# Kernel tuning notes

Measured on AMD Instinct MI355X. Metric: run time of the kernel, lower is better.

## Reference

```python
import jax, jax.numpy as jnp
from jax import lax
import numpy as np

B, H, W, C = 32, 56, 56, 384
NH, WS, SS = 12, 7, 3
HD = C // NH
N = WS * WS
HID = 384  # int(mlp_ratio*dim / reduce_scale) = int(4*384/4)
SCALE = HD ** -0.5
L = H * W


def _rel_pos_index():
    coords = np.stack(np.meshgrid(np.arange(WS), np.arange(WS), indexing='ij'))
    cf = coords.reshape(2, -1)
    rc = (cf[:, :, None] - cf[:, None, :]).transpose(1, 2, 0)
    rc[..., 0] += WS - 1
    rc[..., 1] += WS - 1
    rc[..., 0] *= 2 * WS - 1
    return rc.sum(-1).reshape(-1)  # (N*N,)


def _win_part_np(x):
    b, h, w, c = x.shape
    x = x.reshape(b, h // WS, WS, w // WS, WS, c).transpose(0, 1, 3, 2, 4, 5)
    return x.reshape(-1, WS, WS, c)


def _attn_mask():
    img = np.zeros((1, H, W, 1), np.float32)
    cnt = 0
    sl = (slice(0, -WS), slice(-WS, -SS), slice(-SS, None))
    for hs in sl:
        for ws in sl:
            img[:, hs, ws, :] = cnt
            cnt += 1
    mw = _win_part_np(img).reshape(-1, N)
    am = mw[:, None, :] - mw[:, :, None]
    return np.where(am != 0, -100.0, 0.0).astype(np.float32)  # (nW, N, N)


REL_IDX = _rel_pos_index()
ATTN_MASK = _attn_mask()


def window_partition(x):  # (B,H,W,C) -> (B*nW, N, C)
    x = x.reshape(B, H // WS, WS, W // WS, WS, C).transpose(0, 1, 3, 2, 4, 5)
    return x.reshape(-1, N, C)


def window_reverse(wins):  # (B*nW, N, C) -> (B,H,W,C)
    x = wins.reshape(B, H // WS, W // WS, WS, WS, C).transpose(0, 1, 3, 2, 4, 5)
    return x.reshape(B, H, W, C)


def _ln(x, g, b):
    m = x.mean(-1, keepdims=True)
    v = ((x - m) ** 2).mean(-1, keepdims=True)
    return (x - m) * lax.rsqrt(v + 1e-5) * g + b


def setup_inputs() -> dict:
    key = jax.random.key(0)
    ks = iter(jax.random.split(key, 16))
    w = lambda shape: jax.random.normal(next(ks), shape, jnp.float32) * 0.02
    return {
        'x': jax.random.normal(next(ks), (B, L, C), jnp.float32),
        'norm1_g': jnp.ones((C,), jnp.float32), 'norm1_b': jnp.zeros((C,), jnp.float32),
        'qkv_w': w((3 * C, C)), 'qkv_b': jnp.zeros((3 * C,), jnp.float32),
        'rpb_table': w(((2 * WS - 1) ** 2, NH)),
        'proj_w': w((C, C)), 'proj_b': jnp.zeros((C,), jnp.float32),
        'se1_w': w((C // 2, C)), 'se1_b': jnp.zeros((C // 2,), jnp.float32),
        'se2_w': w((C, C // 2)), 'se2_b': jnp.zeros((C,), jnp.float32),
        'norm2_g': jnp.ones((C,), jnp.float32), 'norm2_b': jnp.zeros((C,), jnp.float32),
        'c1_w': w((HID, C)), 'c1_b': jnp.zeros((HID,), jnp.float32),
        'bn1_g': jnp.ones((HID,), jnp.float32), 'bn1_b': jnp.zeros((HID,), jnp.float32),
        'dw_w': w((HID, 1, 3, 3)), 'dw_b': jnp.zeros((HID,), jnp.float32),
        'bn2_g': jnp.ones((HID,), jnp.float32), 'bn2_b': jnp.zeros((HID,), jnp.float32),
        'c2_w': w((C, HID)), 'c2_b': jnp.zeros((C,), jnp.float32),
        'bn3_g': jnp.ones((C,), jnp.float32), 'bn3_b': jnp.zeros((C,), jnp.float32),
    }


def reference(x, norm1_g, norm1_b, qkv_w, qkv_b, rpb_table, proj_w, proj_b,
              se1_w, se1_b, se2_w, se2_b, norm2_g, norm2_b,
              c1_w, c1_b, bn1_g, bn1_b, dw_w, dw_b, bn2_g, bn2_b,
              c2_w, c2_b, bn3_g, bn3_b):
    shortcut = x
    h = _ln(x, norm1_g, norm1_b).reshape(B, H, W, C)
    h = jnp.roll(h, (-SS, -SS), axis=(1, 2))           # cyclic shift (SW-MSA)
    win = window_partition(h)                            # (B*nW, N, C)
    qkv = (win @ qkv_w.T + qkv_b).reshape(-1, N, 3, NH, HD).transpose(2, 0, 3, 1, 4)
    q, k, v = qkv[0] * SCALE, qkv[1], qkv[2]             # (B*nW, NH, N, HD)
    attn = jnp.einsum('bhnd,bhmd->bhnm', q, k)           # (B*nW, NH, N, N)
    rpb = rpb_table[jnp.asarray(REL_IDX)].reshape(N, N, NH).transpose(2, 0, 1)
    attn = attn + rpb[None]
    mask = jnp.asarray(ATTN_MASK)                        # (nW, N, N)
    nW = mask.shape[0]
    attn = (attn.reshape(B, nW, NH, N, N) + mask[None, :, None]).reshape(-1, NH, N, N)
    attn = jax.nn.softmax(attn, axis=-1)
    out = jnp.einsum('bhnm,bhmd->bhnd', attn, v).transpose(0, 2, 1, 3).reshape(-1, N, C)
    out = out @ proj_w.T + proj_b
    h = window_reverse(out)
    h = jnp.roll(h, (SS, SS), axis=(1, 2)).reshape(B, L, C)
    x = shortcut + h
    # SE gating, applied token-wise over channel dim exactly as ChannelSELayer_SA
    g = jax.nn.relu(x @ se1_w.T + se1_b)
    g = jax.nn.sigmoid(g @ se2_w.T + se2_b)
    x = x * g
    # light conv MLP branch (Mlp_Light); BatchNorm in eval mode with running
    # mean 0 / var 1 -> pure per-channel affine
    y = _ln(x, norm2_g, norm2_b).reshape(B, H, W, C).transpose(0, 3, 1, 2)  # NCHW
    y = jnp.einsum('bchw,oc->bohw', y, c1_w) + c1_b[None, :, None, None]     # 1x1 conv
    y = jax.nn.gelu(y, approximate=False) * bn1_g[None, :, None, None] + bn1_b[None, :, None, None]
    y = lax.conv_general_dilated(y, dw_w, (1, 1), 'SAME', feature_group_count=HID,
                                 dimension_numbers=('NCHW', 'OIHW', 'NCHW')) + dw_b[None, :, None, None]
    y = jax.nn.gelu(y, approximate=False) * bn2_g[None, :, None, None] + bn2_b[None, :, None, None]
    y = jnp.einsum('bchw,oc->bohw', y, c2_w) + c2_b[None, :, None, None]     # 1x1 conv
    y = y * bn3_g[None, :, None, None] + bn3_b[None, :, None, None]
    x = x + y.transpose(0, 2, 3, 1).reshape(B, L, C)
    return x
```

## Files before the change

### kernel.cpp

```cpp
#include <hip/hip_runtime.h>
#include <hip/hip_bf16.h>

typedef __attribute__((ext_vector_type(4))) float f32x4;
typedef __attribute__((ext_vector_type(8))) __bf16 bf16x8;
typedef __attribute__((ext_vector_type(8))) unsigned short u16x8;

#define SCALE_ 0.17677669529663687f
#define RS 19267584

#define OFF_R1 77070336ull
#define OFF_WB 154140672ull
#define OFF_WT 156205056ull

__device__ __forceinline__ __bf16 tobf(float f) {
  __hip_bfloat16 h = __float2bfloat16(f);
  return __builtin_bit_cast(__bf16, h);
}
__device__ __forceinline__ unsigned short f2u(float f) {
  return __builtin_bit_cast(unsigned short, __float2bfloat16(f));
}

__global__ __launch_bounds__(256) void cvt_kernel(const float* __restrict__ src,
                                                  __hip_bfloat16* __restrict__ dst, int n) {
  int i = blockIdx.x * 256 + threadIdx.x;
  int stride = gridDim.x * 256;
  for (; i < n; i += stride) dst[i] = __float2bfloat16(src[i]);
}

__global__ __launch_bounds__(256) void dwrep_kernel(const float* __restrict__ src,
                                                    float* __restrict__ dst) {
  int i = blockIdx.x * 256 + threadIdx.x;
  if (i < 3456) {
    int c = i / 9, k = i - c * 9;
    dst[k * 384 + c] = src[i];
  }
}

template <bool WIN>
__global__ __launch_bounds__(256) void ln_kernel(const float* __restrict__ x,
                                                 const float* __restrict__ gm,
                                                 const float* __restrict__ bt,
                                                 __hip_bfloat16* __restrict__ out) {
  const int tok = blockIdx.x * 4 + (threadIdx.x >> 6);
  const int lane = threadIdx.x & 63;
  const float2* row = (const float2*)(x + (size_t)tok * 384);
  float2 v[3];
  v[0] = row[lane]; v[1] = row[lane + 64]; v[2] = row[lane + 128];
  float s = 0.f, sq = 0.f;
#pragma unroll
  for (int i = 0; i < 3; ++i) { s += v[i].x + v[i].y; sq += v[i].x * v[i].x + v[i].y * v[i].y; }
#pragma unroll
  for (int m = 1; m < 64; m <<= 1) { s += __shfl_xor(s, m, 64); sq += __shfl_xor(sq, m, 64); }
  const float mean = s * (1.f / 384.f);
  const float var = sq * (1.f / 384.f) - mean * mean;
  const float rstd = rsqrtf(var + 1e-5f);
  size_t dst;
  if constexpr (WIN) {
    int b = tok / 3136, l = tok - b * 3136;
    int i = l / 56, j = l - i * 56;
    int hp = i - 3; if (hp < 0) hp += 56;
    int wp = j - 3; if (wp < 0) wp += 56;
    int wi = (hp / 7) * 8 + wp / 7;
    int n = (hp % 7) * 7 + wp % 7;
    dst = (size_t)(b * 64 + wi) * 49 + n;
  } else {
    dst = (size_t)tok;
  }
  unsigned int* o = (unsigned int*)(out + dst * 384);
  const float2* G = (const float2*)gm;
  const float2* Bv = (const float2*)bt;
#pragma unroll
  for (int i = 0; i < 3; ++i) {
    int j = lane + 64 * i;
    float2 gv = G[j], bv = Bv[j];
    float a = (v[i].x - mean) * rstd * gv.x + bv.x;
    float b2 = (v[i].y - mean) * rstd * gv.y + bv.y;
    o[j] = (unsigned)f2u(a) | ((unsigned)f2u(b2) << 16);
  }
}

enum { EPI_PROJ = 0, EPI_SE2 = 2, EPI_C1 = 3, EPI_C2 = 4, EPI_QKV = 5 };

template <int EPI, int KD>
__global__ __launch_bounds__(256) void gemm5(const __hip_bfloat16* __restrict__ Ap,
                                             const __hip_bfloat16* __restrict__ W,
                                             const float* __restrict__ bias,
                                             const float* __restrict__ p0,
                                             const float* __restrict__ p1,
                                             const float* __restrict__ p2,
                                             void* __restrict__ outp) {
  constexpr int KS = KD / 32;
  const int tid = threadIdx.x;
  const int lane = tid & 63, wave = tid >> 6;
  const int g = lane >> 4, r = lane & 15;
  const int row0 = blockIdx.x * 64;
  const int col0 = blockIdx.y * 192;
  const int n0 = wave * 48;

  __shared__ __align__(16) __hip_bfloat16 Al[64][40];
  __shared__ __align__(16) __hip_bfloat16 Bl[192][40];

  const int s_row = tid >> 2, s_c = (tid & 3) * 8;
  const size_t arow = (size_t)(row0 + s_row);

  f32x4 acc[4][3] = {};
  bf16x8 a_reg = *(const bf16x8*)(Ap + arow * KD + s_c);
  bf16x8 b_reg[3];
#pragma unroll
  for (int h = 0; h < 3; ++h)
    b_reg[h] = *(const bf16x8*)(W + (size_t)(col0 + s_row + 64 * h) * KD + s_c);

  for (int kk = 0; kk < KS; ++kk) {
    *(bf16x8*)(&Al[s_row][s_c]) = a_reg;
#pragma unroll
    for (int h = 0; h < 3; ++h) *(bf16x8*)(&Bl[s_row + 64 * h][s_c]) = b_reg[h];
    __syncthreads();
    if (kk + 1 < KS) {
      const int kb = (kk + 1) * 32 + s_c;
      a_reg = *(const bf16x8*)(Ap + arow * KD + kb);
#pragma unroll
      for (int h = 0; h < 3; ++h)
        b_reg[h] = *(const bf16x8*)(W + (size_t)(col0 + s_row + 64 * h) * KD + kb);
    }
    bf16x8 af[4];
#pragma unroll
    for (int mt = 0; mt < 4; ++mt) af[mt] = *(const bf16x8*)(&Al[mt * 16 + r][g * 8]);
#pragma unroll
    for (int nt = 0; nt < 3; ++nt) {
      bf16x8 bf = *(const bf16x8*)(&Bl[n0 + nt * 16 + r][g * 8]);
#pragma unroll
      for (int mt = 0; mt < 4; ++mt)
        acc[mt][nt] = __builtin_amdgcn_mfma_f32_16x16x32_bf16(af[mt], bf, acc[mt][nt], 0, 0, 0);
    }
    __syncthreads();
  }

#pragma unroll
  for (int mt = 0; mt < 4; ++mt) {
#pragma unroll
    for (int j = 0; j < 4; ++j) {
      const int row = row0 + mt * 16 + g * 4 + j;
#pragma unroll
      for (int nt = 0; nt < 3; ++nt) {
        const int col = col0 + n0 + nt * 16 + r;
        float v = acc[mt][nt][j] + bias[col];
        if constexpr (EPI == EPI_QKV) {
          const int s = col / 384, cs = col - s * 384;
          if (s == 0) v *= SCALE_;
          ((__hip_bfloat16*)outp)[(size_t)s * RS + (size_t)row * 384 + cs] = __float2bfloat16(v);
        } else if constexpr (EPI == EPI_C1) {
          float gl = 0.5f * v * (1.f + erff(v * 0.70710678118654752f));
          ((__hip_bfloat16*)outp)[(size_t)row * 384 + col] =
              __float2bfloat16(gl * p0[col] + p1[col]);
        } else {
          float y = v * p0[col] + p1[col];
          ((float*)outp)[(size_t)row * 384 + col] = p2[(size_t)row * 384 + col] + y;
        }
      }
    }
  }
}

template <int EPI, int KD>
__global__ __launch_bounds__(256) void gemm3(const __hip_bfloat16* __restrict__ Ap,
                                             const __hip_bfloat16* __restrict__ W,
                                             const float* __restrict__ bias,
                                             const float* __restrict__ p0,
                                             const float* __restrict__ p1,
                                             const float* __restrict__ p2,
                                             void* __restrict__ outp,
                                             const __hip_bfloat16* __restrict__ W2,
                                             const float* __restrict__ bias2,
                                             void* __restrict__ out2) {
  constexpr int NT = 6;
  constexpr int KS = KD / 32;
  constexpr int LDS_B = (EPI == EPI_SE2) ? 52224 : 50176;
  const int tid = threadIdx.x;
  const int lane = tid & 63, wave = tid >> 6;
  const int g = lane >> 4, r = lane & 15;
  const int row0 = blockIdx.x * 64;
  const int n0 = wave * 96;

  __shared__ __align__(16) char smem[LDS_B];
  auto Al = (__hip_bfloat16(*)[40])smem;
  auto Bl = (__hip_bfloat16(*)[40])(smem + 64 * 80);

  const int s_row = tid >> 2;
  const int s_c = (tid & 3) * 8;

  size_t arow;
  if constexpr (EPI == EPI_PROJ) {
    int t = row0 + s_row;
    int b = t / 3136, l = t - b * 3136;
    int i = l / 56, j = l - i * 56;
    int hp = i >= 3 ? i - 3 : i + 53;
    int wp = j >= 3 ? j - 3 : j + 53;
    arow = ((size_t)(b * 64 + (hp / 7) * 8 + wp / 7)) * 49 + (hp % 7) * 7 + (wp % 7);
  } else {
    arow = (size_t)(row0 + s_row);
  }

  f32x4 acc[4][NT] = {};

  bf16x8 a_reg = *(const bf16x8*)(Ap + arow * KD + s_c);
  bf16x8 b_reg[NT];
#pragma unroll
  for (int h = 0; h < NT; ++h)
    b_reg[h] = *(const bf16x8*)(W + (size_t)(s_row + 64 * h) * KD + s_c);

  for (int kk = 0; kk < KS; ++kk) {
    *(bf16x8*)(&Al[s_row][s_c]) = a_reg;
#pragma unroll
    for (int h = 0; h < NT; ++h) *(bf16x8*)(&Bl[s_row + 64 * h][s_c]) = b_reg[h];
    __syncthreads();
    if (kk + 1 < KS) {
      const int kb = (kk + 1) * 32 + s_c;
      a_reg = *(const bf16x8*)(Ap + arow * KD + kb);
#pragma unroll
      for (int h = 0; h < NT; ++h)
        b_reg[h] = *(const bf16x8*)(W + (size_t)(s_row + 64 * h) * KD + kb);
    }
    bf16x8 af[4];
#pragma unroll
    for (int mt = 0; mt < 4; ++mt) af[mt] = *(const bf16x8*)(&Al[mt * 16 + r][g * 8]);
#pragma unroll
    for (int nt = 0; nt < NT; ++nt) {
      bf16x8 bf = *(const bf16x8*)(&Bl[n0 + nt * 16 + r][g * 8]);
#pragma unroll
      for (int mt = 0; mt < 4; ++mt)
        acc[mt][nt] = __builtin_amdgcn_mfma_f32_16x16x32_bf16(af[mt], bf, acc[mt][nt], 0, 0, 0);
    }
    __syncthreads();
  }

  if constexpr (EPI == EPI_PROJ) {
    auto Xt = (__hip_bfloat16(*)[392])smem;
#pragma unroll
    for (int mt = 0; mt < 4; ++mt)
#pragma unroll
      for (int j = 0; j < 4; ++j) {
        const int lrow = mt * 16 + g * 4 + j;
        const size_t ob = (size_t)(row0 + lrow) * 384;
#pragma unroll
        for (int nt = 0; nt < NT; ++nt) {
          const int col = n0 + nt * 16 + r;
          float v = acc[mt][nt][j] + bias[col] + p0[ob + col];
          ((float*)outp)[ob + col] = v;
          Xt[lrow][col] = __float2bfloat16(v);
        }
      }
    __syncthreads();
    f32x4 acc2[4][3] = {};
    const int c0 = wave * 48;
    for (int kk = 0; kk < 12; ++kk) {
      bf16x8 af2[4];
#pragma unroll
      for (int mt = 0; mt < 4; ++mt)
        af2[mt] = *(const bf16x8*)(&Xt[mt * 16 + r][kk * 32 + g * 8]);
#pragma unroll
      for (int nt2 = 0; nt2 < 3; ++nt2) {
        bf16x8 b2 = *(const bf16x8*)(W2 + (size_t)(c0 + nt2 * 16 + r) * 384 + kk * 32 + g * 8);
#pragma unroll
        for (int mt = 0; mt < 4; ++mt)
          acc2[mt][nt2] = __builtin_amdgcn_mfma_f32_16x16x32_bf16(af2[mt], b2, acc2[mt][nt2], 0, 0, 0);
      }
    }
#pragma unroll
    for (int mt = 0; mt < 4; ++mt)
#pragma unroll
      for (int j = 0; j < 4; ++j) {
        const size_t row = row0 + mt * 16 + g * 4 + j;
#pragma unroll
        for (int nt2 = 0; nt2 < 3; ++nt2) {
          const int col2 = c0 + nt2 * 16 + r;
          float v = acc2[mt][nt2][j] + bias2[col2];
          ((__hip_bfloat16*)out2)[row * 192 + col2] = __float2bfloat16(fmaxf(v, 0.f));
        }
      }
  } else {
    auto Xt = (__hip_bfloat16(*)[392])smem;
    float* st = (float*)(smem + 50176);
#pragma unroll
    for (int mt = 0; mt < 4; ++mt)
#pragma unroll
      for (int j = 0; j < 4; ++j) {
        const int lrow = mt * 16 + g * 4 + j;
        const size_t ob = (size_t)(row0 + lrow) * 384;
        float s = 0.f, sq = 0.f;
#pragma unroll
        for (int nt = 0; nt < NT; ++nt) {
          const int col = n0 + nt * 16 + r;
          float v = acc[mt][nt][j] + bias[col];
          float gate = 1.f / (1.f + __expf(-v));
          float x2 = p0[ob + col] * gate;
          ((float*)outp)[ob + col] = x2;
          Xt[lrow][col] = __float2bfloat16(x2);
          s += x2; sq += x2 * x2;
        }
#pragma unroll
        for (int m = 1; m < 16; m <<= 1) { s += __shfl_xor(s, m, 64); sq += __shfl_xor(sq, m, 64); }
        if (r == 0) { st[wave * 128 + lrow] = s; st[wave * 128 + 64 + lrow] = sq; }
      }
    __syncthreads();
#pragma unroll
    for (int mt = 0; mt < 4; ++mt)
#pragma unroll
      for (int j = 0; j < 4; ++j) {
        const int lrow = mt * 16 + g * 4 + j;
        float sum = st[lrow] + st[128 + lrow] + st[256 + lrow] + st[384 + lrow];
        float ssq = st[64 + lrow] + st[192 + lrow] + st[320 + lrow] + st[448 + lrow];
        float mean = sum * (1.f / 384.f);
        float var = ssq * (1.f / 384.f) - mean * mean;
        float rstd = rsqrtf(var + 1e-5f);
        const size_t row = row0 + lrow;
#pragma unroll
        for (int nt = 0; nt < NT; ++nt) {
          const int col = n0 + nt * 16 + r;
          float xv = __bfloat162float(Xt[lrow][col]);
          float o = (xv - mean) * rstd * p1[col] + p2[col];
          ((__hip_bfloat16*)out2)[row * 384 + col] = __float2bfloat16(o);
        }
      }
  }
}

__global__ __launch_bounds__(64) void attn_core(const __hip_bfloat16* __restrict__ qkv,
                                                const float* __restrict__ rpb,
                                                __hip_bfloat16* __restrict__ ao, int win0) {
  const int bid = blockIdx.x;
  const int win_l = bid / 12, head = bid - win_l * 12;
  const int win = win0 + win_l;
  const int widx = win & 63;
  const int lane = threadIdx.x;
  const int g = lane >> 4, r = lane & 15;
  const int wbh = (widx >> 3) * 7, wbw = (widx & 7) * 7;
  const size_t rowbase = (size_t)(win_l * 49) * 384 + head * 32;
  const __hip_bfloat16* q_g = qkv + rowbase;
  const __hip_bfloat16* k_g = qkv + RS + rowbase;
  const __hip_bfloat16* v_g = qkv + 2 * RS + rowbase;

  __shared__ __align__(16) __hip_bfloat16 P_l[49 * 64];
  __shared__ __align__(16) unsigned short vT[32 * 72];

  bf16x8 zf;
#pragma unroll
  for (int i = 0; i < 8; ++i) zf[i] = tobf(0.f);

  for (int i = lane; i < 512; i += 64) {
    int d = i >> 4, t = 48 + (i & 15);
    vT[d * 72 + t] = 0;
  }
  if (lane < 49) {
#pragma unroll
    for (int c = 0; c < 4; ++c) {
      u16x8 vv = *(const u16x8*)(v_g + (size_t)lane * 384 + c * 8);
#pragma unroll
      for (int e = 0; e < 8; ++e) vT[(c * 8 + e) * 72 + lane] = vv[e];
    }
  }

  int yj4[4], xj4[4], rj4[4];
  bool val4[4];
#pragma unroll
  for (int nt = 0; nt < 4; ++nt) {
    int jt = nt * 16 + r;
    val4[nt] = jt < 49;
    int jc = val4[nt] ? jt : 0;
    int yj = jc / 7, xj = jc - yj * 7;
    yj4[nt] = yj; xj4[nt] = xj;
    int hj = wbh + yj, wj = wbw + xj;
    rj4[nt] = (hj < 49 ? 0 : (hj < 53 ? 1 : 2)) * 3 + (wj < 49 ? 0 : (wj < 53 ? 1 : 2));
  }

  f32x4 sA[4][4] = {};
  {
    bf16x8 qa[4];
#pragma unroll
    for (int mt = 0; mt < 4; ++mt) {
      int row = mt * 16 + r;
      qa[mt] = (row < 49) ? *(const bf16x8*)(q_g + (size_t)row * 384 + g * 8) : zf;
    }
#pragma unroll
    for (int nt = 0; nt < 4; ++nt) {
      int rowk = nt * 16 + r;
      bf16x8 kf = (rowk < 49) ? *(const bf16x8*)(k_g + (size_t)rowk * 384 + g * 8) : zf;
#pragma unroll
      for (int mt = 0; mt < 4; ++mt)
        sA[mt][nt] = __builtin_amdgcn_mfma_f32_16x16x32_bf16(qa[mt], kf, sA[mt][nt], 0, 0, 0);
    }
  }
#pragma unroll
  for (int mt = 0; mt < 4; ++mt) {
#pragma unroll
    for (int j = 0; j < 4; ++j) {
      const int it = mt * 16 + g * 4 + j;
      if (it < 49) {
        int yi = it / 7, xi = it - yi * 7;
        int hi = wbh + yi, wi2 = wbw + xi;
        int ri = (hi < 49 ? 0 : (hi < 53 ? 1 : 2)) * 3 + (wi2 < 49 ? 0 : (wi2 < 53 ? 1 : 2));
        float v4[4];
#pragma unroll
        for (int nt = 0; nt < 4; ++nt) {
          float sv = -1e30f;
          if (val4[nt]) {
            sv = sA[mt][nt][j] + rpb[((yi - yj4[nt] + 6) * 13 + (xi - xj4[nt] + 6)) * 12 + head];
            if (ri != rj4[nt]) sv -= 100.f;
// ... 98 lines not shown
  }
  const int hm = hq > 0 ? hq - 1 : 0;
  const int hp = hq < 55 ? hq + 1 : 55;
  const __hip_bfloat16* r0 = y1 + ((size_t)(b * 3136 + hm * 56)) * 384 + cb;
  const __hip_bfloat16* r1 = y1 + ((size_t)(b * 3136 + hq * 56)) * 384 + cb;
  const __hip_bfloat16* r2 = y1 + ((size_t)(b * 3136 + hp * 56)) * 384 + cb;
  __hip_bfloat16* op = y2 + ((size_t)(b * 3136 + hq * 56)) * 384 + cb;

  u16x8 zv;
#pragma unroll
  for (int i = 0; i < 8; ++i) zv[i] = 0;
#define LDC(rp, x) (((unsigned)(x) < 56u) ? *(const u16x8*)((rp) + (size_t)(x) * 384) : zv)

  u16x8 L0 = LDC(r0, x0 - 1), L1 = LDC(r1, x0 - 1), L2 = LDC(r2, x0 - 1);
  u16x8 C0 = LDC(r0, x0), C1 = LDC(r1, x0), C2 = LDC(r2, x0);
#pragma unroll
  for (int xi = 0; xi < 14; ++xi) {
    const int x = x0 + xi;
    u16x8 R0 = LDC(r0, x + 1), R1 = LDC(r1, x + 1), R2 = LDC(r2, x + 1);
    float acc[8];
#pragma unroll
    for (int i = 0; i < 8; ++i) acc[i] = bias[i];
#pragma unroll
    for (int i = 0; i < 8; ++i) {
      acc[i] += __uint_as_float((unsigned)L0[i] << 16) * wr[0][i];
      acc[i] += __uint_as_float((unsigned)C0[i] << 16) * wr[1][i];
      acc[i] += __uint_as_float((unsigned)R0[i] << 16) * wr[2][i];
      acc[i] += __uint_as_float((unsigned)L1[i] << 16) * wr[3][i];
      acc[i] += __uint_as_float((unsigned)C1[i] << 16) * wr[4][i];
      acc[i] += __uint_as_float((unsigned)R1[i] << 16) * wr[5][i];
      acc[i] += __uint_as_float((unsigned)L2[i] << 16) * wr[6][i];
      acc[i] += __uint_as_float((unsigned)C2[i] << 16) * wr[7][i];
      acc[i] += __uint_as_float((unsigned)R2[i] << 16) * wr[8][i];
    }
    u16x8 o;
#pragma unroll
    for (int i = 0; i < 8; ++i) {
      float u = acc[i];
      float gl = 0.5f * u * (1.f + erff(u * 0.70710678118654752f));
      o[i] = f2u(gl * gv[i] + bv[i]);
    }
    *(u16x8*)(op + (size_t)x * 384) = o;
    L0 = C0; L1 = C1; L2 = C2;
    C0 = R0; C1 = R1; C2 = R2;
  }
#undef LDC
}

extern "C" void kernel_launch(void* const* d_in, const int* in_sizes, int n_in, void* d_out,
                              int out_size, void* d_ws, size_t ws_size, hipStream_t stream) {
  (void)in_sizes; (void)n_in; (void)out_size; (void)ws_size;
  const float* x = (const float*)d_in[0];
  const float* n1g = (const float*)d_in[1];
  const float* n1b = (const float*)d_in[2];
  const float* qkv_w = (const float*)d_in[3];
  const float* qkv_b = (const float*)d_in[4];
  const float* rpb = (const float*)d_in[5];
  const float* proj_w = (const float*)d_in[6];
  const float* proj_b = (const float*)d_in[7];
  const float* se1_w = (const float*)d_in[8];
  const float* se1_b = (const float*)d_in[9];
  const float* se2_w = (const float*)d_in[10];
  const float* se2_b = (const float*)d_in[11];
  const float* n2g = (const float*)d_in[12];
  const float* n2b = (const float*)d_in[13];
  const float* c1_w = (const float*)d_in[14];
  const float* c1_b = (const float*)d_in[15];
  const float* bn1g = (const float*)d_in[16];
  const float* bn1b = (const float*)d_in[17];
  const float* dw_w = (const float*)d_in[18];
  const float* dw_b = (const float*)d_in[19];
  const float* bn2g = (const float*)d_in[20];
  const float* bn2b = (const float*)d_in[21];
  const float* c2_w = (const float*)d_in[22];
  const float* c2_b = (const float*)d_in[23];
  const float* bn3g = (const float*)d_in[24];
  const float* bn3b = (const float*)d_in[25];

  char* ws = (char*)d_ws;
  __hip_bfloat16* r0b = (__hip_bfloat16*)ws;
  __hip_bfloat16* r1b = (__hip_bfloat16*)(ws + OFF_R1);
  __hip_bfloat16* wbp = (__hip_bfloat16*)(ws + OFF_WB);
  float* wt = (float*)(ws + OFF_WT);
  __hip_bfloat16* qkv_wb = wbp;
  __hip_bfloat16* proj_wb = wbp + 442368;
  __hip_bfloat16* se1_wb = wbp + 589824;
  __hip_bfloat16* se2_wb = wbp + 663552;
  __hip_bfloat16* c1_wb = wbp + 737280;
  __hip_bfloat16* c2_wb = wbp + 884736;
  float* out = (float*)d_out;

  cvt_kernel<<<1728, 256, 0, stream>>>(qkv_w, qkv_wb, 442368);
  cvt_kernel<<<576, 256, 0, stream>>>(proj_w, proj_wb, 147456);
  cvt_kernel<<<288, 256, 0, stream>>>(se1_w, se1_wb, 73728);
  cvt_kernel<<<288, 256, 0, stream>>>(se2_w, se2_wb, 73728);
  cvt_kernel<<<576, 256, 0, stream>>>(c1_w, c1_wb, 147456);
  cvt_kernel<<<576, 256, 0, stream>>>(c2_w, c2_wb, 147456);
  dwrep_kernel<<<14, 256, 0, stream>>>(dw_w, wt);

  ln_kernel<true><<<25088, 256, 0, stream>>>(x, n1g, n1b, r0b);

  for (int c = 0; c < 2; ++c) {
    const __hip_bfloat16* xa = r0b + (size_t)c * 50176 * 384;
    gemm5<EPI_QKV, 384><<<dim3(784, 6), 256, 0, stream>>>(
        xa, qkv_wb, qkv_b, nullptr, nullptr, nullptr, out);
    attn_core<<<12288, 64, 0, stream>>>((const __hip_bfloat16*)out, rpb, r0b, c * 1024);
  }

  gemm3<EPI_PROJ, 384><<<1568, 256, 0, stream>>>(
      r0b, proj_wb, proj_b, x, nullptr, nullptr, out, se1_wb, se1_b, r1b);
  gemm3<EPI_SE2, 192><<<1568, 256, 0, stream>>>(
      r1b, se2_wb, se2_b, out, n2g, n2b, out, nullptr, nullptr, r0b);
  gemm5<EPI_C1, 384><<<dim3(1568, 2), 256, 0, stream>>>(
      r0b, c1_wb, c1_b, bn1g, bn1b, nullptr, r1b);
  dw_kernel<<<1344, 256, 0, stream>>>(r1b, wt, dw_b, bn2g, bn2b, r0b);
  gemm5<EPI_C2, 384><<<dim3(1568, 2), 256, 0, stream>>>(
      r0b, c2_wb, c2_b, bn3g, bn3b, out, out);
}
```

Measured before the change: 957.5 us.

## Fuse proj, SE gating and LayerNorm2 into a single mega kernel

Merges the proj GEMM (with residual add), SE1/SE2 GEMMs, sigmoid gating and the second LayerNorm into one kernel that keeps the 64-row tile in registers and LDS. This drops the intermediate fp32 write/read of the post-proj activation and the SE hidden-buffer round trip, and removes one kernel launch. Buffer roles for the later conv stages are swapped to match. The trade-off is higher register pressure from holding the proj accumulators across the SE stages, which may lower occupancy.

```diff
diff --git a/kernel.cpp b/kernel.cpp
--- a/kernel.cpp
+++ b/kernel.cpp
@@ -79,7 +79,7 @@
   }
 }
 
-enum { EPI_PROJ = 0, EPI_SE2 = 2, EPI_C1 = 3, EPI_C2 = 4, EPI_QKV = 5 };
+enum { EPI_C1 = 3, EPI_C2 = 4, EPI_QKV = 5 };
 
 template <int EPI, int KD>
 __global__ __launch_bounds__(256) void gemm5(const __hip_bfloat16* __restrict__ Ap,
@@ -161,70 +161,64 @@
   }
 }
 
-template <int EPI, int KD>
-__global__ __launch_bounds__(256) void gemm3(const __hip_bfloat16* __restrict__ Ap,
-                                             const __hip_bfloat16* __restrict__ W,
-                                             const float* __restrict__ bias,
-                                             const float* __restrict__ p0,
-                                             const float* __restrict__ p1,
-                                             const float* __restrict__ p2,
-                                             void* __restrict__ outp,
-                                             const __hip_bfloat16* __restrict__ W2,
-                                             const float* __restrict__ bias2,
-                                             void* __restrict__ out2) {
-  constexpr int NT = 6;
-  constexpr int KS = KD / 32;
-  constexpr int LDS_B = (EPI == EPI_SE2) ? 52224 : 50176;
+__global__ __launch_bounds__(256) void mega_kernel(const __hip_bfloat16* __restrict__ ao,
+                                                   const __hip_bfloat16* __restrict__ Wp,
+                                                   const float* __restrict__ bp,
+                                                   const float* __restrict__ x,
+                                                   const __hip_bfloat16* __restrict__ W1,
+                                                   const float* __restrict__ b1,
+                                                   const __hip_bfloat16* __restrict__ W2se,
+                                                   const float* __restrict__ b2se,
+                                                   const float* __restrict__ lng,
+                                                   const float* __restrict__ lnb,
+                                                   float* __restrict__ x2out,
+                                                   __hip_bfloat16* __restrict__ ln2out) {
   const int tid = threadIdx.x;
   const int lane = tid & 63, wave = tid >> 6;
   const int g = lane >> 4, r = lane & 15;
   const int row0 = blockIdx.x * 64;
   const int n0 = wave * 96;
 
-  __shared__ __align__(16) char smem[LDS_B];
+  __shared__ __align__(16) char smem[50176];
   auto Al = (__hip_bfloat16(*)[40])smem;
-  auto Bl = (__hip_bfloat16(*)[40])(smem + 64 * 80);
+  auto Bl = (__hip_bfloat16(*)[40])(smem + 5120);
 
   const int s_row = tid >> 2;
   const int s_c = (tid & 3) * 8;
 
   size_t arow;
-  if constexpr (EPI == EPI_PROJ) {
+  {
     int t = row0 + s_row;
     int b = t / 3136, l = t - b * 3136;
     int i = l / 56, j = l - i * 56;
     int hp = i >= 3 ? i - 3 : i + 53;
     int wp = j >= 3 ? j - 3 : j + 53;
     arow = ((size_t)(b * 64 + (hp / 7) * 8 + wp / 7)) * 49 + (hp % 7) * 7 + (wp % 7);
-  } else {
-    arow = (size_t)(row0 + s_row);
-  }
-
-  f32x4 acc[4][NT] = {};
-
-  bf16x8 a_reg = *(const bf16x8*)(Ap + arow * KD + s_c);
-  bf16x8 b_reg[NT];
-#pragma unroll
-  for (int h = 0; h < NT; ++h)
-    b_reg[h] = *(const bf16x8*)(W + (size_t)(s_row + 64 * h) * KD + s_c);
-
-  for (int kk = 0; kk < KS; ++kk) {
+  }
+
+  f32x4 acc[4][6] = {};
+  bf16x8 a_reg = *(const bf16x8*)(ao + arow * 384 + s_c);
+  bf16x8 b_reg[6];
+#pragma unroll
+  for (int h = 0; h < 6; ++h)
+    b_reg[h] = *(const bf16x8*)(Wp + (size_t)(s_row + 64 * h) * 384 + s_c);
+  for (int kk = 0; kk < 12; ++kk) {
     *(bf16x8*)(&Al[s_row][s_c]) = a_reg;
 #pragma unroll
-    for (int h = 0; h < NT; ++h) *(bf16x8*)(&Bl[s_row + 64 * h][s_c]) = b_reg[h];
+    for (int h = 0; h < 6; ++h) *(bf16x8*)(&Bl[s_row + 64 * h][s_c]) = b_reg[h];
     __syncthreads();
-    if (kk + 1 < KS) {
+    if (kk + 1 < 12) {
       const int kb = (kk + 1) * 32 + s_c;
-      a_reg = *(const bf16x8*)(Ap + arow * KD + kb);
-#pragma unroll
-      for (int h = 0; h < NT; ++h)
-        b_reg[h] = *(const bf16x8*)(W + (size_t)(s_row + 64 * h) * KD + kb);
+      a_reg = *(const bf16x8*)(ao + arow * 384 + kb);
+#pragma unroll
+      for (int h = 0; h < 6; ++h)
+        b_reg[h] = *(const bf16x8*)(Wp + (size_t)(s_row + 64 * h) * 384 + kb);
     }
     bf16x8 af[4];
 #pragma unroll
     for (int mt = 0; mt < 4; ++mt) af[mt] = *(const bf16x8*)(&Al[mt * 16 + r][g * 8]);
 #pragma unroll
-    for (int nt = 0; nt < NT; ++nt) {
+    for (int nt = 0; nt < 6; ++nt) {
       bf16x8 bf = *(const bf16x8*)(&Bl[n0 + nt * 16 + r][g * 8]);
 #pragma unroll
       for (int mt = 0; mt < 4; ++mt)
@@ -233,8 +227,70 @@
     __syncthreads();
   }
 
-  if constexpr (EPI == EPI_PROJ) {
-    auto Xt = (__hip_bfloat16(*)[392])smem;
+  auto Xt = (__hip_bfloat16(*)[392])smem;
+#pragma unroll
+  for (int mt = 0; mt < 4; ++mt)
+#pragma unroll
+    for (int j = 0; j < 4; ++j) {
+      const int lrow = mt * 16 + g * 4 + j;
+      const size_t ob = (size_t)(row0 + lrow) * 384;
+#pragma unroll
+      for (int nt = 0; nt < 6; ++nt) {
+        const int col = n0 + nt * 16 + r;
+        float v = acc[mt][nt][j] + bp[col] + x[ob + col];
+        acc[mt][nt][j] = v;
+        Xt[lrow][col] = __float2bfloat16(v);
+      }
+    }
+  __syncthreads();
+
+  f32x4 acc2[4][3] = {};
+  const int c0 = wave * 48;
+  for (int kk = 0; kk < 12; ++kk) {
+    bf16x8 af2[4];
+#pragma unroll
+    for (int mt = 0; mt < 4; ++mt)
+      af2[mt] = *(const bf16x8*)(&Xt[mt * 16 + r][kk * 32 + g * 8]);
+#pragma unroll
+    for (int nt2 = 0; nt2 < 3; ++nt2) {
+      bf16x8 b2 = *(const bf16x8*)(W1 + (size_t)(c0 + nt2 * 16 + r) * 384 + kk * 32 + g * 8);
+#pragma unroll
+      for (int mt = 0; mt < 4; ++mt)
+        acc2[mt][nt2] = __builtin_amdgcn_mfma_f32_16x16x32_bf16(af2[mt], b2, acc2[mt][nt2], 0, 0, 0);
+    }
+  }
+  __syncthreads();
+  auto G1 = (__hip_bfloat16(*)[200])smem;
+#pragma unroll
+  for (int mt = 0; mt < 4; ++mt)
+#pragma unroll
+    for (int j = 0; j < 4; ++j) {
+      const int lrow = mt * 16 + g * 4 + j;
+#pragma unroll
+      for (int nt2 = 0; nt2 < 3; ++nt2) {
+        const int col2 = c0 + nt2 * 16 + r;
+        G1[lrow][col2] = __float2bfloat16(fmaxf(acc2[mt][nt2][j] + b1[col2], 0.f));
+      }
+    }
+  __syncthreads();
+
+#pragma unroll
+  for (int h = 0; h < 2; ++h) {
+    f32x4 acc3[4][3] = {};
+    for (int kk = 0; kk < 6; ++kk) {
+      bf16x8 af3[4];
+#pragma unroll
+      for (int mt = 0; mt < 4; ++mt)
+        af3[mt] = *(const bf16x8*)(&G1[mt * 16 + r][kk * 32 + g * 8]);
+#pragma unroll
+      for (int nt = 0; nt < 3; ++nt) {
+        const int col = n0 + h * 48 + nt * 16 + r;
+        bf16x8 b3 = *(const bf16x8*)(W2se + (size_t)col * 192 + kk * 32 + g * 8);
+#pragma unroll
+        for (int mt = 0; mt < 4; ++mt)
+          acc3[mt][nt] = __builtin_amdgcn_mfma_f32_16x16x32_bf16(af3[mt], b3, acc3[mt][nt], 0, 0, 0);
+      }
+    }
 #pragma unroll
     for (int mt = 0; mt < 4; ++mt)
 #pragma unroll
@@ -242,86 +298,51 @@
         const int lrow = mt * 16 + g * 4 + j;
         const size_t ob = (size_t)(row0 + lrow) * 384;
 #pragma unroll
-        for (int nt = 0; nt < NT; ++nt) {
-          const int col = n0 + nt * 16 + r;
-          float v = acc[mt][nt][j] + bias[col] + p0[ob + col];
-          ((float*)outp)[ob + col] = v;
-          Xt[lrow][col] = __float2bfloat16(v);
+        for (int nt = 0; nt < 3; ++nt) {
+          const int col = n0 + h * 48 + nt * 16 + r;
+          float gate = 1.f / (1.f + __expf(-(acc3[mt][nt][j] + b2se[col])));
+          float x2 = acc[mt][h * 3 + nt][j] * gate;
+          acc[mt][h * 3 + nt][j] = x2;
+          x2out[ob + col] = x2;
         }
       }
-    __syncthreads();
-    f32x4 acc2[4][3] = {};
-    const int c0 = wave * 48;
-    for (int kk = 0; kk < 12; ++kk) {
-      bf16x8 af2[4];
-#pragma unroll
-      for (int mt = 0; mt < 4; ++mt)
-        af2[mt] = *(const bf16x8*)(&Xt[mt * 16 + r][kk * 32 + g * 8]);
-#pragma unroll
-      for (int nt2 = 0; nt2 < 3; ++nt2) {
-        bf16x8 b2 = *(const bf16x8*)(W2 + (size_t)(c0 + nt2 * 16 + r) * 384 + kk * 32 + g * 8);
-#pragma unroll
-        for (int mt = 0; mt < 4; ++mt)
-          acc2[mt][nt2] = __builtin_amdgcn_mfma_f32_16x16x32_bf16(af2[mt], b2, acc2[mt][nt2], 0, 0, 0);
-      }
-    }
-#pragma unroll
-    for (int mt = 0; mt < 4; ++mt)
-#pragma unroll
-      for (int j = 0; j < 4; ++j) {
-        const size_t row = row0 + mt * 16 + g * 4 + j;
-#pragma unroll
-        for (int nt2 = 0; nt2 < 3; ++nt2) {
-          const int col2 = c0 + nt2 * 16 + r;
-          float v = acc2[mt][nt2][j] + bias2[col2];
-          ((__hip_bfloat16*)out2)[row * 192 + col2] = __float2bfloat16(fmaxf(v, 0.f));
-        }
-      }
-  } else {
-    auto Xt = (__hip_bfloat16(*)[392])smem;
-    float* st = (float*)(smem + 50176);
-#pragma unroll
-    for (int mt = 0; mt < 4; ++mt)
-#pragma unroll
-      for (int j = 0; j < 4; ++j) {
-        const int lrow = mt * 16 + g * 4 + j;
-        const size_t ob = (size_t)(row0 + lrow) * 384;
-        float s = 0.f, sq = 0.f;
-#pragma unroll
-        for (int nt = 0; nt < NT; ++nt) {
-          const int col = n0 + nt * 16 + r;
-          float v = acc[mt][nt][j] + bias[col];
-          float gate = 1.f / (1.f + __expf(-v));
-          float x2 = p0[ob + col] * gate;
-          ((float*)outp)[ob + col] = x2;
-          Xt[lrow][col] = __float2bfloat16(x2);
-          s += x2; sq += x2 * x2;
-        }
-#pragma unroll
-        for (int m = 1; m < 16; m <<= 1) { s += __shfl_xor(s, m, 64); sq += __shfl_xor(sq, m, 64); }
-        if (r == 0) { st[wave * 128 + lrow] = s; st[wave * 128 + 64 + lrow] = sq; }
-      }
-    __syncthreads();
-#pragma unroll
-    for (int mt = 0; mt < 4; ++mt)
-#pragma unroll
-      for (int j = 0; j < 4; ++j) {
-        const int lrow = mt * 16 + g * 4 + j;
-        float sum = st[lrow] + st[128 + lrow] + st[256 + lrow] + st[384 + lrow];
-        float ssq = st[64 + lrow] + st[192 + lrow] + st[320 + lrow] + st[448 + lrow];
-        float mean = sum * (1.f / 384.f);
-        float var = ssq * (1.f / 384.f) - mean * mean;
-        float rstd = rsqrtf(var + 1e-5f);
-        const size_t row = row0 + lrow;
-#pragma unroll
-        for (int nt = 0; nt < NT; ++nt) {
-          const int col = n0 + nt * 16 + r;
-          float xv = __bfloat162float(Xt[lrow][col]);
-          float o = (xv - mean) * rstd * p1[col] + p2[col];
-          ((__hip_bfloat16*)out2)[row * 384 + col] = __float2bfloat16(o);
-        }
-      }
-  }
+  }
+
+  float* st = (float*)(smem + 25600);
+#pragma unroll
+  for (int mt = 0; mt < 4; ++mt)
+#pragma unroll
+    for (int j = 0; j < 4; ++j) {
+      const int lrow = mt * 16 + g * 4 + j;
+      float s = 0.f, sq = 0.f;
+#pragma unroll
+      for (int nt = 0; nt < 6; ++nt) {
+        float v = acc[mt][nt][j];
+        s += v; sq += v * v;
+      }
+#pragma unroll
+      for (int m = 1; m < 16; m <<= 1) { s += __shfl_xor(s, m, 64); sq += __shfl_xor(sq, m, 64); }
+      if (r == 0) { st[wave * 128 + lrow] = s; st[wave * 128 + 64 + lrow] = sq; }
+    }
+  __syncthreads();
+#pragma unroll
+  for (int mt = 0; mt < 4; ++mt)
+#pragma unroll
+    for (int j = 0; j < 4; ++j) {
+      const int lrow = mt * 16 + g * 4 + j;
+      float sum = st[lrow] + st[128 + lrow] + st[256 + lrow] + st[384 + lrow];
+      float ssq = st[64 + lrow] + st[192 + lrow] + st[320 + lrow] + st[448 + lrow];
+      float mean = sum * (1.f / 384.f);
+      float var = ssq * (1.f / 384.f) - mean * mean;
+      float rstd = rsqrtf(var + 1e-5f);
+      const size_t row = row0 + lrow;
+#pragma unroll
+      for (int nt = 0; nt < 6; ++nt) {
+        const int col = n0 + nt * 16 + r;
+        float o = (acc[mt][nt][j] - mean) * rstd * lng[col] + lnb[col];
+        ln2out[row * 384 + col] = __float2bfloat16(o);
+      }
+    }
 }
 
 __global__ __launch_bounds__(64) void attn_core(const __hip_bfloat16* __restrict__ qkv,
@@ -611,13 +632,11 @@
     attn_core<<<12288, 64, 0, stream>>>((const __hip_bfloat16*)out, rpb, r0b, c * 1024);
   }
 
-  gemm3<EPI_PROJ, 384><<<1568, 256, 0, stream>>>(
-      r0b, proj_wb, proj_b, x, nullptr, nullptr, out, se1_wb, se1_b, r1b);
-  gemm3<EPI_SE2, 192><<<1568, 256, 0, stream>>>(
-      r1b, se2_wb, se2_b, out, n2g, n2b, out, nullptr, nullptr, r0b);
+  mega_kernel<<<1568, 256, 0, stream>>>(r0b, proj_wb, proj_b, x, se1_wb, se1_b, se2_wb, se2_b,
+                                        n2g, n2b, out, r1b);
   gemm5<EPI_C1, 384><<<dim3(1568, 2), 256, 0, stream>>>(
-      r0b, c1_wb, c1_b, bn1g, bn1b, nullptr, r1b);
-  dw_kernel<<<1344, 256, 0, stream>>>(r1b, wt, dw_b, bn2g, bn2b, r0b);
+      r1b, c1_wb, c1_b, bn1g, bn1b, nullptr, r0b);
+  dw_kernel<<<1344, 256, 0, stream>>>(r0b, wt, dw_b, bn2g, bn2b, r1b);
   gemm5<EPI_C2, 384><<<dim3(1568, 2), 256, 0, stream>>>(
-      r0b, c2_wb, c2_b, bn3g, bn3b, out, out);
-}
+      r1b, c2_wb, c2_b, bn3g, bn3b, out, out);
+}
```

Result: slower. 1.117 ms (+16.6%).

## Fold LayerNorm2 into conv1 GEMM weights and simplify SE2 epilogue

Applied to the files above, without the earlier changes.

LayerNorm2 is folded algebraically into the first 1x1 conv. Its gamma is premultiplied into the conv weights, and its beta is folded into the bias. The per-row mean and rstd are computed inside the new conv kernel, which reads the fp32 SE output directly and applies the correction in the epilogue. The SE2 GEMM becomes a plain gemm5 with a sigmoid-gate epilogue and no longer writes the normalized bf16 tensor, which removes one intermediate write and read. In exchange, the conv kernel rereads the fp32 activations for its statistics and converts them to bf16 on the fly, and folding gamma into bf16 weights may change numerics slightly.

```diff
diff --git a/kernel.cpp b/kernel.cpp
--- a/kernel.cpp
+++ b/kernel.cpp
@@ -11,6 +11,7 @@
 #define OFF_R1 77070336ull
 #define OFF_WB 154140672ull
 #define OFF_WT 156205056ull
+#define OFF_SB 156218880ull
 
 __device__ __forceinline__ __bf16 tobf(float f) {
   __hip_bfloat16 h = __float2bfloat16(f);
@@ -34,6 +35,28 @@
     int c = i / 9, k = i - c * 9;
     dst[k * 384 + c] = src[i];
   }
+}
+
+__global__ __launch_bounds__(256) void c1prep_kernel(const float* __restrict__ c1w,
+                                                     const float* __restrict__ c1b,
+                                                     const float* __restrict__ g,
+                                                     const float* __restrict__ b,
+                                                     __hip_bfloat16* __restrict__ gc1,
+                                                     float* __restrict__ S1,
+                                                     float* __restrict__ bb) {
+  const int n = blockIdx.x * 4 + (threadIdx.x >> 6);
+  const int lane = threadIdx.x & 63;
+  float s1 = 0.f, sb = 0.f;
+  for (int k = lane; k < 384; k += 64) {
+    float w = c1w[n * 384 + k];
+    __hip_bfloat16 gw = __float2bfloat16(w * g[k]);
+    gc1[n * 384 + k] = gw;
+    s1 += __bfloat162float(gw);
+    sb += w * b[k];
+  }
+#pragma unroll
+  for (int m = 1; m < 64; m <<= 1) { s1 += __shfl_xor(s1, m, 64); sb += __shfl_xor(sb, m, 64); }
+  if (lane == 0) { S1[n] = s1; bb[n] = c1b[n] + sb; }
 }
 
 template <bool WIN>
@@ -79,7 +102,7 @@
   }
 }
 
-enum { EPI_PROJ = 0, EPI_SE2 = 2, EPI_C1 = 3, EPI_C2 = 4, EPI_QKV = 5 };
+enum { EPI_SE2 = 2, EPI_C2 = 4, EPI_QKV = 5 };
 
 template <int EPI, int KD>
 __global__ __launch_bounds__(256) void gemm5(const __hip_bfloat16* __restrict__ Ap,
@@ -148,10 +171,9 @@
           const int s = col / 384, cs = col - s * 384;
           if (s == 0) v *= SCALE_;
           ((__hip_bfloat16*)outp)[(size_t)s * RS + (size_t)row * 384 + cs] = __float2bfloat16(v);
-        } else if constexpr (EPI == EPI_C1) {
-          float gl = 0.5f * v * (1.f + erff(v * 0.70710678118654752f));
-          ((__hip_bfloat16*)outp)[(size_t)row * 384 + col] =
-              __float2bfloat16(gl * p0[col] + p1[col]);
+        } else if constexpr (EPI == EPI_SE2) {
+          float gate = 1.f / (1.f + __expf(-v));
+          ((float*)outp)[(size_t)row * 384 + col] = p0[(size_t)row * 384 + col] * gate;
         } else {
           float y = v * p0[col] + p1[col];
           ((float*)outp)[(size_t)row * 384 + col] = p2[(size_t)row * 384 + col] + y;
@@ -161,27 +183,123 @@
   }
 }
 
-template <int EPI, int KD>
-__global__ __launch_bounds__(256) void gemm3(const __hip_bfloat16* __restrict__ Ap,
-                                             const __hip_bfloat16* __restrict__ W,
-                                             const float* __restrict__ bias,
-                                             const float* __restrict__ p0,
-                                             const float* __restrict__ p1,
-                                             const float* __restrict__ p2,
-                                             void* __restrict__ outp,
-                                             const __hip_bfloat16* __restrict__ W2,
-                                             const float* __restrict__ bias2,
-                                             void* __restrict__ out2) {
+__global__ __launch_bounds__(256) void c1ln_kernel(const float* __restrict__ x2,
+                                                   const __hip_bfloat16* __restrict__ gc1,
+                                                   const float* __restrict__ S1,
+                                                   const float* __restrict__ bb,
+                                                   const float* __restrict__ bn1g_,
+                                                   const float* __restrict__ bn1b_,
+                                                   __hip_bfloat16* __restrict__ y1) {
+  const int tid = threadIdx.x;
+  const int lane = tid & 63, wave = tid >> 6;
+  const int g = lane >> 4, r = lane & 15;
+  const int row0 = blockIdx.x * 64;
+  const int col0 = blockIdx.y * 192;
+  const int n0 = wave * 48;
+
+  __shared__ __align__(16) __hip_bfloat16 Al[64][40];
+  __shared__ __align__(16) __hip_bfloat16 Bl[192][40];
+  __shared__ float mean_l[64], rstd_l[64];
+
+  const int s_row = tid >> 2, s_c = (tid & 3) * 8;
+  const size_t abase = (size_t)(row0 + s_row) * 384;
+
+  {
+    float s = 0.f, sq = 0.f;
+#pragma unroll
+    for (int c = 0; c < 12; ++c) {
+      const float4* p = (const float4*)(x2 + abase + c * 32 + s_c);
+      float4 a = p[0], b = p[1];
+      s += a.x + a.y + a.z + a.w + b.x + b.y + b.z + b.w;
+      sq += a.x * a.x + a.y * a.y + a.z * a.z + a.w * a.w +
+            b.x * b.x + b.y * b.y + b.z * b.z + b.w * b.w;
+    }
+#pragma unroll
+    for (int m = 1; m < 4; m <<= 1) { s += __shfl_xor(s, m, 64); sq += __shfl_xor(sq, m, 64); }
+    if ((tid & 3) == 0) {
+      float mean = s * (1.f / 384.f);
+      float var = sq * (1.f / 384.f) - mean * mean;
+      mean_l[s_row] = mean;
+      rstd_l[s_row] = rsqrtf(var + 1e-5f);
+    }
+  }
+  __syncthreads();
+
+  f32x4 acc[4][3] = {};
+  bf16x8 a_reg;
+  {
+    const float4* sp = (const float4*)(x2 + abase + s_c);
+    float4 a = sp[0], b = sp[1];
+    a_reg[0] = tobf(a.x); a_reg[1] = tobf(a.y); a_reg[2] = tobf(a.z); a_reg[3] = tobf(a.w);
+    a_reg[4] = tobf(b.x); a_reg[5] = tobf(b.y); a_reg[6] = tobf(b.z); a_reg[7] = tobf(b.w);
+  }
+  bf16x8 b_reg[3];
+#pragma unroll
+  for (int h = 0; h < 3; ++h)
+    b_reg[h] = *(const bf16x8*)(gc1 + (size_t)(col0 + s_row + 64 * h) * 384 + s_c);
+
+  for (int kk = 0; kk < 12; ++kk) {
+    *(bf16x8*)(&Al[s_row][s_c]) = a_reg;
+#pragma unroll
+    for (int h = 0; h < 3; ++h) *(bf16x8*)(&Bl[s_row + 64 * h][s_c]) = b_reg[h];
+    __syncthreads();
+    if (kk + 1 < 12) {
+      const int kb = (kk + 1) * 32 + s_c;
+      const float4* sp = (const float4*)(x2 + abase + kb);
+      float4 a = sp[0], b = sp[1];
+      a_reg[0] = tobf(a.x); a_reg[1] = tobf(a.y); a_reg[2] = tobf(a.z); a_reg[3] = tobf(a.w);
+      a_reg[4] = tobf(b.x); a_reg[5] = tobf(b.y); a_reg[6] = tobf(b.z); a_reg[7] = tobf(b.w);
+#pragma unroll
+      for (int h = 0; h < 3; ++h)
+        b_reg[h] = *(const bf16x8*)(gc1 + (size_t)(col0 + s_row + 64 * h) * 384 + kb);
+    }
+    bf16x8 af[4];
+#pragma unroll
+    for (int mt = 0; mt < 4; ++mt) af[mt] = *(const bf16x8*)(&Al[mt * 16 + r][g * 8]);
+#pragma unroll
+    for (int nt = 0; nt < 3; ++nt) {
+      bf16x8 bf = *(const bf16x8*)(&Bl[n0 + nt * 16 + r][g * 8]);
+#pragma unroll
+      for (int mt = 0; mt < 4; ++mt)
+        acc[mt][nt] = __builtin_amdgcn_mfma_f32_16x16x32_bf16(af[mt], bf, acc[mt][nt], 0, 0, 0);
+    }
+    __syncthreads();
+  }
+
+#pragma unroll
+  for (int mt = 0; mt < 4; ++mt) {
+#pragma unroll
+    for (int j = 0; j < 4; ++j) {
+      const int rl = mt * 16 + g * 4 + j;
+      const int row = row0 + rl;
+      const float mean = mean_l[rl], rstd = rstd_l[rl];
+#pragma unroll
+      for (int nt = 0; nt < 3; ++nt) {
+        const int col = col0 + n0 + nt * 16 + r;
+        float v = rstd * (acc[mt][nt][j] - mean * S1[col]) + bb[col];
+        float gl = 0.5f * v * (1.f + erff(v * 0.70710678118654752f));
+        y1[(size_t)row * 384 + col] = __float2bfloat16(gl * bn1g_[col] + bn1b_[col]);
+      }
+    }
+  }
+}
+
+__global__ __launch_bounds__(256) void gemm3_proj(const __hip_bfloat16* __restrict__ Ap,
+                                                  const __hip_bfloat16* __restrict__ W,
+                                                  const float* __restrict__ bias,
+                                                  const float* __restrict__ p0,
+                                                  void* __restrict__ outp,
+                                                  const __hip_bfloat16* __restrict__ W2,
+                                                  const float* __restrict__ bias2,
+                                                  void* __restrict__ out2) {
   constexpr int NT = 6;
-  constexpr int KS = KD / 32;
-  constexpr int LDS_B = (EPI == EPI_SE2) ? 52224 : 50176;
   const int tid = threadIdx.x;
   const int lane = tid & 63, wave = tid >> 6;
   const int g = lane >> 4, r = lane & 15;
   const int row0 = blockIdx.x * 64;
   const int n0 = wave * 96;
 
-  __shared__ __align__(16) char smem[LDS_B];
+  __shared__ __align__(16) char smem[50176];
   auto Al = (__hip_bfloat16(*)[40])smem;
   auto Bl = (__hip_bfloat16(*)[40])(smem + 64 * 80);
 
@@ -189,36 +307,34 @@
   const int s_c = (tid & 3) * 8;
 
   size_t arow;
-  if constexpr (EPI == EPI_PROJ) {
+  {
     int t = row0 + s_row;
     int b = t / 3136, l = t - b * 3136;
     int i = l / 56, j = l - i * 56;
     int hp = i >= 3 ? i - 3 : i + 53;
     int wp = j >= 3 ? j - 3 : j + 53;
     arow = ((size_t)(b * 64 + (hp / 7) * 8 + wp / 7)) * 49 + (hp % 7) * 7 + (wp % 7);
-  } else {
-    arow = (size_t)(row0 + s_row);
   }
 
   f32x4 acc[4][NT] = {};
 
-  bf16x8 a_reg = *(const bf16x8*)(Ap + arow * KD + s_c);
+  bf16x8 a_reg = *(const bf16x8*)(Ap + arow * 384 + s_c);
   bf16x8 b_reg[NT];
 #pragma unroll
   for (int h = 0; h < NT; ++h)
-    b_reg[h] = *(const bf16x8*)(W + (size_t)(s_row + 64 * h) * KD + s_c);
-
-  for (int kk = 0; kk < KS; ++kk) {
+    b_reg[h] = *(const bf16x8*)(W + (size_t)(s_row + 64 * h) * 384 + s_c);
+
+  for (int kk = 0; kk < 12; ++kk) {
     *(bf16x8*)(&Al[s_row][s_c]) = a_reg;
 #pragma unroll
     for (int h = 0; h < NT; ++h) *(bf16x8*)(&Bl[s_row + 64 * h][s_c]) = b_reg[h];
     __syncthreads();
-    if (kk + 1 < KS) {
+    if (kk + 1 < 12) {
       const int kb = (kk + 1) * 32 + s_c;
-      a_reg = *(const bf16x8*)(Ap + arow * KD + kb);
+      a_reg = *(const bf16x8*)(Ap + arow * 384 + kb);
 #pragma unroll
       for (int h = 0; h < NT; ++h)
-        b_reg[h] = *(const bf16x8*)(W + (size_t)(s_row + 64 * h) * KD + kb);
+        b_reg[h] = *(const bf16x8*)(W + (size_t)(s_row + 64 * h) * 384 + kb);
     }
     bf16x8 af[4];
 #pragma unroll
@@ -233,95 +349,49 @@
     __syncthreads();
   }
 
-  if constexpr (EPI == EPI_PROJ) {
-    auto Xt = (__hip_bfloat16(*)[392])smem;
+  auto Xt = (__hip_bfloat16(*)[392])smem;
+#pragma unroll
+  for (int mt = 0; mt < 4; ++mt)
+#pragma unroll
+    for (int j = 0; j < 4; ++j) {
+      const int lrow = mt * 16 + g * 4 + j;
+      const size_t ob = (size_t)(row0 + lrow) * 384;
+#pragma unroll
+      for (int nt = 0; nt < NT; ++nt) {
+        const int col = n0 + nt * 16 + r;
+        float v = acc[mt][nt][j] + bias[col] + p0[ob + col];
+        ((float*)outp)[ob + col] = v;
+        Xt[lrow][col] = __float2bfloat16(v);
+      }
+    }
+  __syncthreads();
+  f32x4 acc2[4][3] = {};
+  const int c0 = wave * 48;
+  for (int kk = 0; kk < 12; ++kk) {
+    bf16x8 af2[4];
 #pragma unroll
     for (int mt = 0; mt < 4; ++mt)
-#pragma unroll
-      for (int j = 0; j < 4; ++j) {
-        const int lrow = mt * 16 + g * 4 + j;
-        const size_t ob = (size_t)(row0 + lrow) * 384;
-#pragma unroll
-        for (int nt = 0; nt < NT; ++nt) {
-          const int col = n0 + nt * 16 + r;
-          float v = acc[mt][nt][j] + bias[col] + p0[ob + col];
-          ((float*)outp)[ob + col] = v;
-          Xt[lrow][col] = __float2bfloat16(v);
-        }
+      af2[mt] = *(const bf16x8*)(&Xt[mt * 16 + r][kk * 32 + g * 8]);
+#pragma unroll
+    for (int nt2 = 0; nt2 < 3; ++nt2) {
+      bf16x8 b2 = *(const bf16x8*)(W2 + (size_t)(c0 + nt2 * 16 + r) * 384 + kk * 32 + g * 8);
+#pragma unroll
+      for (int mt = 0; mt < 4; ++mt)
+        acc2[mt][nt2] = __builtin_amdgcn_mfma_f32_16x16x32_bf16(af2[mt], b2, acc2[mt][nt2], 0, 0, 0);
+    }
+  }
+#pragma unroll
+  for (int mt = 0; mt < 4; ++mt)
+#pragma unroll
+    for (int j = 0; j < 4; ++j) {
+      const size_t row = row0 + mt * 16 + g * 4 + j;
+#pragma unroll
+      for (int nt2 = 0; nt2 < 3; ++nt2) {
+        const int col2 = c0 + nt2 * 16 + r;
+        float v = acc2[mt][nt2][j] + bias2[col2];
+        ((__hip_bfloat16*)out2)[row * 192 + col2] = __float2bfloat16(fmaxf(v, 0.f));
       }
-    __syncthreads();
-    f32x4 acc2[4][3] = {};
-    const int c0 = wave * 48;
-    for (int kk = 0; kk < 12; ++kk) {
-      bf16x8 af2[4];
-#pragma unroll
-      for (int mt = 0; mt < 4; ++mt)
-        af2[mt] = *(const bf16x8*)(&Xt[mt * 16 + r][kk * 32 + g * 8]);
-#pragma unroll
-      for (int nt2 = 0; nt2 < 3; ++nt2) {
-        bf16x8 b2 = *(const bf16x8*)(W2 + (size_t)(c0 + nt2 * 16 + r) * 384 + kk * 32 + g * 8);
-#pragma unroll
-        for (int mt = 0; mt < 4; ++mt)
-          acc2[mt][nt2] = __builtin_amdgcn_mfma_f32_16x16x32_bf16(af2[mt], b2, acc2[mt][nt2], 0, 0, 0);
-      }
-    }
-#pragma unroll
-    for (int mt = 0; mt < 4; ++mt)
-#pragma unroll
-      for (int j = 0; j < 4; ++j) {
-        const size_t row = row0 + mt * 16 + g * 4 + j;
-#pragma unroll
-        for (int nt2 = 0; nt2 < 3; ++nt2) {
-          const int col2 = c0 + nt2 * 16 + r;
-          float v = acc2[mt][nt2][j] + bias2[col2];
-          ((__hip_bfloat16*)out2)[row * 192 + col2] = __float2bfloat16(fmaxf(v, 0.f));
-        }
-      }
-  } else {
-    auto Xt = (__hip_bfloat16(*)[392])smem;
-    float* st = (float*)(smem + 50176);
-#pragma unroll
-    for (int mt = 0; mt < 4; ++mt)
-#pragma unroll
-      for (int j = 0; j < 4; ++j) {
-        const int lrow = mt * 16 + g * 4 + j;
-        const size_t ob = (size_t)(row0 + lrow) * 384;
-        float s = 0.f, sq = 0.f;
-#pragma unroll
-        for (int nt = 0; nt < NT; ++nt) {
-          const int col = n0 + nt * 16 + r;
-          float v = acc[mt][nt][j] + bias[col];
-          float gate = 1.f / (1.f + __expf(-v));
-          float x2 = p0[ob + col] * gate;
-          ((float*)outp)[ob + col] = x2;
-          Xt[lrow][col] = __float2bfloat16(x2);
-          s += x2; sq += x2 * x2;
-        }
-#pragma unroll
-        for (int m = 1; m < 16; m <<= 1) { s += __shfl_xor(s, m, 64); sq += __shfl_xor(sq, m, 64); }
-        if (r == 0) { st[wave * 128 + lrow] = s; st[wave * 128 + 64 + lrow] = sq; }
-      }
-    __syncthreads();
-#pragma unroll
-    for (int mt = 0; mt < 4; ++mt)
-#pragma unroll
-      for (int j = 0; j < 4; ++j) {
-        const int lrow = mt * 16 + g * 4 + j;
-        float sum = st[lrow] + st[128 + lrow] + st[256 + lrow] + st[384 + lrow];
-        float ssq = st[64 + lrow] + st[192 + lrow] + st[320 + lrow] + st[448 + lrow];
-        float mean = sum * (1.f / 384.f);
-        float var = ssq * (1.f / 384.f) - mean * mean;
-        float rstd = rsqrtf(var + 1e-5f);
-        const size_t row = row0 + lrow;
-#pragma unroll
-        for (int nt = 0; nt < NT; ++nt) {
-          const int col = n0 + nt * 16 + r;
-          float xv = __bfloat162float(Xt[lrow][col]);
-          float o = (xv - mean) * rstd * p1[col] + p2[col];
-          ((__hip_bfloat16*)out2)[row * 384 + col] = __float2bfloat16(o);
-        }
-      }
-  }
+    }
 }
 
 __global__ __launch_bounds__(64) void attn_core(const __hip_bfloat16* __restrict__ qkv,
@@ -586,11 +656,13 @@
   __hip_bfloat16* r1b = (__hip_bfloat16*)(ws + OFF_R1);
   __hip_bfloat16* wbp = (__hip_bfloat16*)(ws + OFF_WB);
   float* wt = (float*)(ws + OFF_WT);
+  float* S1 = (float*)(ws + OFF_SB);
+  float* bb = S1 + 384;
   __hip_bfloat16* qkv_wb = wbp;
   __hip_bfloat16* proj_wb = wbp + 442368;
   __hip_bfloat16* se1_wb = wbp + 589824;
   __hip_bfloat16* se2_wb = wbp + 663552;
-  __hip_bfloat16* c1_wb = wbp + 737280;
+  __hip_bfloat16* gc1 = wbp + 737280;
   __hip_bfloat16* c2_wb = wbp + 884736;
   float* out = (float*)d_out;
 
@@ -598,8 +670,8 @@
   cvt_kernel<<<576, 256, 0, stream>>>(proj_w, proj_wb, 147456);
   cvt_kernel<<<288, 256, 0, stream>>>(se1_w, se1_wb, 73728);
   cvt_kernel<<<288, 256, 0, stream>>>(se2_w, se2_wb, 73728);
-  cvt_kernel<<<576, 256, 0, stream>>>(c1_w, c1_wb, 147456);
   cvt_kernel<<<576, 256, 0, stream>>>(c2_w, c2_wb, 147456);
+  c1prep_kernel<<<96, 256, 0, stream>>>(c1_w, c1_b, n2g, n2b, gc1, S1, bb);
   dwrep_kernel<<<14, 256, 0, stream>>>(dw_w, wt);
 
   ln_kernel<true><<<25088, 256, 0, stream>>>(x, n1g, n1b, r0b);
@@ -611,12 +683,10 @@
     attn_core<<<12288, 64, 0, stream>>>((const __hip_bfloat16*)out, rpb, r0b, c * 1024);
   }
 
-  gemm3<EPI_PROJ, 384><<<1568, 256, 0, stream>>>(
-      r0b, proj_wb, proj_b, x, nullptr, nullptr, out, se1_wb, se1_b, r1b);
-  gemm3<EPI_SE2, 192><<<1568, 256, 0, stream>>>(
-      r1b, se2_wb, se2_b, out, n2g, n2b, out, nullptr, nullptr, r0b);
-  gemm5<EPI_C1, 384><<<dim3(1568, 2), 256, 0, stream>>>(
-      r0b, c1_wb, c1_b, bn1g, bn1b, nullptr, r1b);
+  gemm3_proj<<<1568, 256, 0, stream>>>(r0b, proj_wb, proj_b, x, out, se1_wb, se1_b, r1b);
+  gemm5<EPI_SE2, 192><<<dim3(1568, 2), 256, 0, stream>>>(
+      r1b, se2_wb, se2_b, out, nullptr, nullptr, out);
+  c1ln_kernel<<<dim3(1568, 2), 256, 0, stream>>>(out, gc1, S1, bb, bn1g, bn1b, r1b);
   dw_kernel<<<1344, 256, 0, stream>>>(r1b, wt, dw_b, bn2g, bn2b, r0b);
   gemm5<EPI_C2, 384><<<dim3(1568, 2), 256, 0, stream>>>(
       r0b, c2_wb, c2_b, bn3g, bn3b, out, out);
```

After: 924.5 us. 3.4% less time.
